# Kernel tuning notes

Measured on AMD Instinct MI355X. Metric: run time of the kernel, lower is better.

The kernel has to match this reference:

```python
import jax, jax.numpy as jnp
import numpy as np

HIDDEN = 1024
HEADS = 16
HEAD_DIM = HIDDEN // HEADS
B, T = 4, 2048


def setup_inputs() -> dict:
    key = jax.random.key(0)
    k_x, k_w1, k_b1, k_w2, k_b2 = jax.random.split(key, 5)
    lim1 = 1.0 / np.sqrt(HIDDEN)
    x = jax.random.normal(k_x, (B, T, HIDDEN), dtype=jnp.float32)
    # causal lower-triangular mask, broadcastable to [B, H, T, T]
    mask = jnp.tril(jnp.ones((T, T), dtype=jnp.int32))[None, None, :, :]
    # qkv_proj: Linear(HIDDEN, 3*HIDDEN); torch Linear: y = x @ W.T + b
    W_qkv = jax.random.uniform(k_w1, (3 * HIDDEN, HIDDEN), minval=-lim1, maxval=lim1, dtype=jnp.float32)
    b_qkv = jax.random.uniform(k_b1, (3 * HIDDEN,), minval=-lim1, maxval=lim1, dtype=jnp.float32)
    W_out = jax.random.uniform(k_w2, (HIDDEN, HIDDEN), minval=-lim1, maxval=lim1, dtype=jnp.float32)
    b_out = jax.random.uniform(k_b2, (HIDDEN,), minval=-lim1, maxval=lim1, dtype=jnp.float32)
    return {"x": x, "mask": mask, "W_qkv": W_qkv, "b_qkv": b_qkv, "W_out": W_out, "b_out": b_out}


def reference(x, mask, W_qkv, b_qkv, W_out, b_out):
    Bx, Tx, C = x.shape
    qkv = x @ W_qkv.T + b_qkv                      # [B, T, 3C]
    qkv = qkv.reshape(Bx, Tx, 3, HEADS, HEAD_DIM)
    qkv = jnp.transpose(qkv, (2, 0, 3, 1, 4))      # [3, B, H, T, Dh]
    Q, K, V = qkv[0], qkv[1], qkv[2]
    scale = 1.0 / np.sqrt(HEAD_DIM)
    scores = jnp.einsum('bhqd,bhkd->bhqk', Q, K) * scale  # [B, H, T, T]
    scores = jnp.where(mask == 0, -jnp.inf, scores)
    probs = jax.nn.softmax(scores, axis=-1)
    ctx = jnp.einsum('bhqk,bhkd->bhqd', probs, V)  # [B, H, T, Dh]
    ctx = jnp.transpose(ctx, (0, 2, 1, 3)).reshape(Bx, Tx, C)
    return ctx @ W_out.T + b_out
```

## Files before the change

### kernel.cpp

```cpp
#include <hip/hip_runtime.h>
#include <cstdint>
#include <cstddef>

#define B_ 4
#define T_ 2048
#define C_ 1024
#define H_ 16
#define D_ 64

typedef __attribute__((ext_vector_type(8))) __bf16 bf16x8;
typedef __attribute__((ext_vector_type(4))) float floatx4;

#define QSCL (0.125f * 1.44269504088896f)
#define FMAX 24.0f

__device__ __forceinline__ unsigned short f2bf(float f) {
  union { float f; unsigned int u; } v; v.f = f;
  unsigned int r = v.u + 0x7fffu + ((v.u >> 16) & 1u);
  return (unsigned short)(r >> 16);
}
__device__ __forceinline__ ushort4 pk4(float a, float b, float c, float d) {
  ushort4 u; u.x = f2bf(a); u.y = f2bf(b); u.z = f2bf(c); u.w = f2bf(d);
  return u;
}
__device__ __forceinline__ bf16x8 cvt8(float4 a, float4 b) {
  bf16x8 r;
  r[0] = a.x; r[1] = a.y; r[2] = a.z; r[3] = a.w;
  r[4] = b.x; r[5] = b.y; r[6] = b.z; r[7] = b.w;
  return r;
}
__device__ __forceinline__ unsigned pkbf2(float a, float b) {
  union { __bf16 h[2]; unsigned u; } w;
  w.h[0] = (__bf16)a; w.h[1] = (__bf16)b;
  return w.u;
}

__device__ __forceinline__ void gl_lds16(const void* g, void* l) {
  __builtin_amdgcn_global_load_lds(
      (const __attribute__((address_space(1))) unsigned int*)g,
      (__attribute__((address_space(3))) unsigned int*)l, 16, 0, 0);
}

__global__ __launch_bounds__(256)
void conv_bf16(const float* __restrict__ src, unsigned short* __restrict__ dst,
               int n8) {
  for (int i = blockIdx.x * 256 + threadIdx.x; i < n8; i += gridDim.x * 256) {
    const float4* s = (const float4*)src + 2 * (size_t)i;
    float4 a = s[0], b = s[1];
    ((bf16x8*)dst)[i] = cvt8(a, b);
  }
}

__global__ __launch_bounds__(256)
void conv_tri(const float* __restrict__ s1, unsigned short* __restrict__ d1, int n1,
              const float* __restrict__ s2, unsigned short* __restrict__ d2, int n2,
              const float* __restrict__ s3, unsigned short* __restrict__ d3, int n3) {
  for (int i = blockIdx.x * 256 + threadIdx.x; i < n1 + n2 + n3; i += gridDim.x * 256) {
    const float4* sp; bf16x8* dp;
    if (i < n1)           { sp = (const float4*)s1 + 2 * (size_t)i;       dp = (bf16x8*)d1 + i; }
    else if (i < n1 + n2) { int j = i - n1;      sp = (const float4*)s2 + 2 * (size_t)j; dp = (bf16x8*)d2 + j; }
    else                  { int j = i - n1 - n2; sp = (const float4*)s3 + 2 * (size_t)j; dp = (bf16x8*)d3 + j; }
    float4 a = sp[0], b = sp[1];
    *dp = cvt8(a, b);
  }
}

template<int EPI, int GATHER, int WBF>
__global__ __launch_bounds__(256, 2)
void gemm_bt(const unsigned short* __restrict__ Abf,
             const void* __restrict__ Wraw,
             const float* __restrict__ bias,
             float* __restrict__ out,
             unsigned short* __restrict__ qws,
             unsigned short* __restrict__ kws,
             unsigned short* __restrict__ vtws)
{
  alignas(16) __shared__ unsigned short As[2][128 * 64];
  alignas(16) __shared__ unsigned short Bs[2][WBF ? 128 * 64 : 128 * 72];
  const int tid  = threadIdx.x;
  const int lane = tid & 63;
  const int wid  = tid >> 6;
  const int col  = lane & 15;
  const int quad = lane >> 4;
  const int wm = (wid >> 1) << 6;
  const int wn = (wid & 1) << 6;
  const int bm = blockIdx.y << 7;
  const int bn = blockIdx.x << 7;

  const float* Wf          = (const float*)Wraw;
  const unsigned short* Wb = (const unsigned short*)Wraw;

  const int r0 = tid >> 3;
  const int c0 = tid & 7;

  floatx4 acc[4][4];
#pragma unroll
  for (int i = 0; i < 4; ++i)
#pragma unroll
    for (int j = 0; j < 4; ++j)
      acc[i][j] = (floatx4){0.f, 0.f, 0.f, 0.f};

#define GSTAGE(k0_, nb_)                                                      \
  do {                                                                        \
    _Pragma("unroll") for (int s = 0; s < 4; ++s) {                           \
      const int row  = (s << 5) + r0;                             \
      const int colE = ((c0 ^ (row & 7)) << 3);             \
      const unsigned short* gsrc;                                             \
      if (GATHER) {                                                           \
        const int m = bm + row;                                               \
        const int b = m >> 11, t = m & 2047;                                  \
        const int hh = (k0_) >> 6;                        \
        gsrc = Abf + ((((size_t)(b * 16 + hh) << 11) + t) << 6) + colE;       \
      } else {                                                                \
        gsrc = Abf + (size_t)(bm + row) * 1024 + (k0_) + colE;                \
      }                                                                       \
      gl_lds16(gsrc, (char*)&As[nb_][0] + (s << 12) + (wid << 10));           \
      if (WBF) {                                                              \
        const unsigned short* ws2 = Wb + (size_t)(bn + row) * 1024 + (k0_) + colE; \
        gl_lds16(ws2, (char*)&Bs[nb_][0] + (s << 12) + (wid << 10));          \
      } else {                                                                \
        const int kc = c0 << 3;                                               \
        const float* wsrc = &Wf[(size_t)(bn + row) * 1024 + (k0_) + kc];      \
        float4 w0 = *(const float4*)wsrc;                                     \
        float4 w1 = *(const float4*)(wsrc + 4);                               \
        *(bf16x8*)&Bs[nb_][row * 72 + kc] = cvt8(w0, w1);                     \
      }                                                                       \
    }                                                                         \
  } while (0)

  GSTAGE(0, 0);
  __syncthreads();

  for (int kt = 0; kt < 16; ++kt) {
    const int buf = kt & 1;
    if (kt + 1 < 16) GSTAGE((kt + 1) << 6, buf ^ 1);

#pragma unroll
    for (int kk = 0; kk < 64; kk += 32) {
      bf16x8 af[4], bfr[4];
#pragma unroll
      for (int i = 0; i < 4; ++i) {
        const int r = wm + i * 16 + col;
        af[i] = *(const bf16x8*)&As[buf][(r << 6) + ((kk + quad * 8) ^ ((r & 7) << 3))];
      }
#pragma unroll
      for (int j = 0; j < 4; ++j) {
        const int r = wn + j * 16 + col;
        if (WBF)
          bfr[j] = *(const bf16x8*)&Bs[buf][(r << 6) + ((kk + quad * 8) ^ ((r & 7) << 3))];
        else
          bfr[j] = *(const bf16x8*)&Bs[buf][r * 72 + kk + quad * 8];
      }
#pragma unroll
      for (int i = 0; i < 4; ++i)
#pragma unroll
        for (int j = 0; j < 4; ++j)
          acc[i][j] = __builtin_amdgcn_mfma_f32_16x16x32_bf16(af[i], bfr[j], acc[i][j], 0, 0, 0);
    }

    __syncthreads();
  }
#undef GSTAGE

#pragma unroll
  for (int i = 0; i < 4; ++i) {
    const int row = bm + wm + i * 16 + quad * 4;
#pragma unroll
    for (int j = 0; j < 4; ++j) {
      const int n  = bn + wn + j * 16 + col;
      const float bv = bias[n];
      float v[4];
#pragma unroll
      for (int r = 0; r < 4; ++r) v[r] = acc[i][j][r] + bv;

      if (EPI == 1) {
#pragma unroll
        for (int r = 0; r < 4; ++r)
          out[(size_t)(row + r) * 1024 + n] = v[r];
      } else {
        const int s   = n >> 10;
        const int rem = n & 1023;
        const int h   = rem >> 6;
        const int d   = rem & 63;
        const int b   = row >> 11;
        const int t   = row & 2047;
        const size_t bh = (size_t)(b * H_ + h);
        if (s == 0) {
#pragma unroll
          for (int r = 0; r < 4; ++r)
            qws[(bh * T_ + t + r) * D_ + d] = f2bf(v[r] * QSCL);
        } else if (s == 1) {
#pragma unroll
          for (int r = 0; r < 4; ++r)
            kws[(bh * T_ + t + r) * D_ + d] = f2bf(v[r]);
        } else {
          *(ushort4*)&vtws[(bh * D_ + d) * T_ + t] = pk4(v[0], v[1], v[2], v[3]);
        }
      }
    }
  }
}

__global__ __launch_bounds__(256, 2)
void attn_causal(unsigned short* __restrict__ qws,
                 const unsigned short* __restrict__ kws,
                 const unsigned short* __restrict__ vtws)
{
  alignas(16) __shared__ unsigned short Ks[2][64 * 64];
  alignas(16) __shared__ unsigned short Vs[2][64 * 64];
  const int tid  = threadIdx.x;
  const int lane = tid & 63;
  const int wid  = tid >> 6;
  const int col  = lane & 15;
  const int quad = lane >> 4;

  const int bh   = blockIdx.x & 63;
  const int band = 7 - (blockIdx.x >> 6);

  const unsigned short* Kp  = kws + (size_t)bh * T_ * D_;
  const unsigned short* Vtp = vtws + (size_t)bh * D_ * T_;

  bf16x8 vones;
#pragma unroll
  for (int i = 0; i < 8; ++i) vones[i] = (__bf16)1.0f;

  const int srow8 = lane >> 3;
  const int swz   = ((lane & 7) ^ srow8) << 3;

#define STAGE(kt_, b_)                                                        \
  do {                                                                        \
    _Pragma("unroll") for (int c2 = 0; c2 < 2; ++c2) {                        \
      const int cb = wid + (c2 << 2);                   \
      gl_lds16(Kp + ((size_t)(((kt_) << 6) + (cb << 3) + srow8) << 6) + swz,  \
               (char*)&Ks[b_][0] + (cb << 10));                               \
      gl_lds16(Vtp + ((size_t)((cb << 3) + srow8) << 11) + ((kt_) << 6) + swz,\
               (char*)&Vs[b_][0] + (cb << 10));                               \
    }                                                                         \
  } while (0)

  const int nk    = (band + 1) << 2;
  const int kdiag = (band << 2) + wid;
  const int q0    = (band << 8) + (wid << 6);
  unsigned short* Qp = qws + ((size_t)bh * T_ + q0) * D_;

  bf16x8 bq[4][2];
#pragma unroll
  for (int h = 0; h < 4; ++h) {
    bq[h][0] = *(const bf16x8*)&Qp[(h * 16 + col) * D_ + quad * 8];
    bq[h][1] = *(const bf16x8*)&Qp[(h * 16 + col) * D_ + 32 + quad * 8];
  }

  floatx4 o[4][4], ol[4];
#pragma unroll
  for (int h = 0; h < 4; ++h) {
    ol[h] = (floatx4){0.f, 0.f, 0.f, 0.f};
#pragma unroll
    for (int j = 0; j < 4; ++j) o[h][j] = (floatx4){0.f, 0.f, 0.f, 0.f};
  }

  STAGE(0, 0);
  __syncthreads();

  for (int kt = 0; kt < nk; ++kt) {
    const int buf = kt & 1;
    if (kt + 1 < nk) STAGE(kt + 1, buf ^ 1);

    if (kt <= kdiag) {
      const unsigned short* Kb = &Ks[buf][0];
      bf16x8 kA[4], kB[4];
#pragma unroll
      for (int g = 0; g < 4; ++g) {
        const int r = g * 16 + col;
        kA[g] = *(const bf16x8*)&Kb[(r << 6) + ((quad ^ (col & 7)) << 3)];
        kB[g] = *(const bf16x8*)&Kb[(r << 6) + (((quad | 4) ^ (col & 7)) << 3)];
      }
      const unsigned short* Vb = &Vs[buf][0];
      bf16x8 vA[4], vB[4];
#pragma unroll
      for (int j = 0; j < 4; ++j) {
        const int r = j * 16 + col;
        vA[j] = *(const bf16x8*)&Vb[(r << 6) + ((quad ^ (col & 7)) << 3)];
        vB[j] = *(const bf16x8*)&Vb[(r << 6) + (((quad | 4) ^ (col & 7)) << 3)];
      }

#pragma unroll
      for (int hp = 0; hp < 2; ++hp) {
        floatx4 s[2][4];
        __builtin_amdgcn_s_setprio(1);
#pragma unroll
        for (int hh = 0; hh < 2; ++hh) {
          const int h = hp * 2 + hh;
#pragma unroll
          for (int g = 0; g < 4; ++g) {
            s[hh][g] = (floatx4){-FMAX, -FMAX, -FMAX, -FMAX};
            s[hh][g] = __builtin_amdgcn_mfma_f32_16x16x32_bf16(kA[g], bq[h][0], s[hh][g], 0, 0, 0);
            s[hh][g] = __builtin_amdgcn_mfma_f32_16x16x32_bf16(kB[g], bq[h][1], s[hh][g], 0, 0, 0);
          }
        }
        __builtin_amdgcn_s_setprio(0);

        if (kt == kdiag) {
#pragma unroll
          for (int hh = 0; hh < 2; ++hh) {
            const int lim = ((hp * 2 + hh) << 4) + col;
#pragma unroll
            for (int g = 0; g < 4; ++g)
#pragma unroll
              for (int r = 0; r < 4; ++r)
                if (g * 16 + quad * 4 + r > lim) s[hh][g][r] = -1e30f;
          }
        }

#pragma unroll
        for (int hh = 0; hh < 2; ++hh)
#pragma unroll
          for (int g = 0; g < 4; ++g)
#pragma unroll
            for (int r = 0; r < 4; ++r)
              s[hh][g][r] = __builtin_amdgcn_exp2f(s[hh][g][r]);

        __builtin_amdgcn_s_setprio(1);
#pragma unroll
        for (int hh = 0; hh < 2; ++hh) {
          const int h = hp * 2 + hh;
          unsigned dw[4][2];
#pragma unroll
          for (int g = 0; g < 4; ++g) {
            dw[g][0] = pkbf2(s[hh][g][0], s[hh][g][1]);
            dw[g][1] = pkbf2(s[hh][g][2], s[hh][g][3]);
          }
          unsigned aw[4], bw[4];
          {
            auto t = __builtin_amdgcn_permlane32_swap(dw[0][0], dw[1][0], false, false);
            auto u = __builtin_amdgcn_permlane16_swap(t[0], t[1], false, false);
            aw[0] = u[0]; aw[2] = u[1];
          }
          {
            auto t = __builtin_amdgcn_permlane32_swap(dw[0][1], dw[1][1], false, false);
            auto u = __builtin_amdgcn_permlane16_swap(t[0], t[1], false, false);
            aw[1] = u[0]; aw[3] = u[1];
          }
          {
            auto t = __builtin_amdgcn_permlane32_swap(dw[2][0], dw[3][0], false, false);
            auto u = __builtin_amdgcn_permlane16_swap(t[0], t[1], false, false);
            bw[0] = u[0]; bw[2] = u[1];
          }
          {
            auto t = __builtin_amdgcn_permlane32_swap(dw[2][1], dw[3][1], false, false);
            auto u = __builtin_amdgcn_permlane16_swap(t[0], t[1], false, false);
            bw[1] = u[0]; bw[3] = u[1];
          }
          union { unsigned u[4]; bf16x8 v; } pa0, pa1;
#pragma unroll
          for (int w = 0; w < 4; ++w) { pa0.u[w] = aw[w]; pa1.u[w] = bw[w]; }

#pragma unroll
          for (int j = 0; j < 4; ++j) {
            o[h][j] = __builtin_amdgcn_mfma_f32_16x16x32_bf16(pa0.v, vA[j], o[h][j], 0, 0, 0);
            o[h][j] = __builtin_amdgcn_mfma_f32_16x16x32_bf16(pa1.v, vB[j], o[h][j], 0, 0, 0);
          }
          ol[h] = __builtin_amdgcn_mfma_f32_16x16x32_bf16(pa0.v, vones, ol[h], 0, 0, 0);
          ol[h] = __builtin_amdgcn_mfma_f32_16x16x32_bf16(pa1.v, vones, ol[h], 0, 0, 0);
        }
        __builtin_amdgcn_s_setprio(0);
      }
    }

    __syncthreads();
  }

#pragma unroll
  for (int h = 0; h < 4; ++h) {
    float lr[4];
#pragma unroll
    for (int r = 0; r < 4; ++r) lr[r] = 1.0f / ol[h][r];
#pragma unroll
    for (int j = 0; j < 4; ++j)
#pragma unroll
      for (int r = 0; r < 4; ++r)
        Qp[(size_t)(h * 16 + quad * 4 + r) * D_ + j * 16 + col] =
            f2bf(o[h][j][r] * lr[r]);
  }
#undef STAGE
}

extern "C" void kernel_launch(void* const* d_in, const int* in_sizes, int n_in,
                              void* d_out, int out_size, void* d_ws, size_t ws_size,
                              hipStream_t stream) {
  const float* x     = (const float*)d_in[0];
  const float* W_qkv = (const float*)d_in[2];
  const float* b_qkv = (const float*)d_in[3];
  const float* W_out = (const float*)d_in[4];
  const float* b_out = (const float*)d_in[5];
  float* out = (float*)d_out;

  const size_t per = (size_t)B_ * H_ * T_ * D_;
  unsigned short* qws  = (unsigned short*)d_ws;
  unsigned short* vtws = qws + per;
  unsigned short* kws  = (unsigned short*)d_out;
  unsigned short* xbf  = kws + per;

  const bool bigws  = ws_size >= (size_t)38 * 1024 * 1024;
  const bool hugews = ws_size >= (size_t)40 * 1024 * 1024;
  unsigned short* wqbf = vtws + per;
  unsigned short* wobf = wqbf + (size_t)3 * C_ * C_;

  if (hugews) {
    conv_tri<<<dim3(2048), 256, 0, stream>>>(
        x, xbf, (int)(per >> 3),
        W_qkv, wqbf, (3 * C_ * C_) >> 3,
        W_out, wobf, (C_ * C_) >> 3);
    gemm_bt<0, 0, 1><<<dim3(3072 / 128, 8192 / 128), 256, 0, stream>>>(
        xbf, (const void*)wqbf, b_qkv, nullptr, qws, kws, vtws);
  } else if (bigws) {
    conv_tri<<<dim3(2048), 256, 0, stream>>>(
        x, xbf, (int)(per >> 3),
        W_qkv, wqbf, (3 * C_ * C_) >> 3,
        nullptr, nullptr, 0);
    gemm_bt<0, 0, 1><<<dim3(3072 / 128, 8192 / 128), 256, 0, stream>>>(
        xbf, (const void*)wqbf, b_qkv, nullptr, qws, kws, vtws);
  } else {
    conv_bf16<<<dim3(2048), 256, 0, stream>>>(x, xbf, (int)(per >> 3));
    gemm_bt<0, 0, 0><<<dim3(3072 / 128, 8192 / 128), 256, 0, stream>>>(
        xbf, (const void*)W_qkv, b_qkv, nullptr, qws, kws, vtws);
  }

  attn_causal<<<dim3(8 * 64), 256, 0, stream>>>(qws, kws, vtws);

  if (hugews) {
    gemm_bt<1, 1, 1><<<dim3(1024 / 128, 8192 / 128), 256, 0, stream>>>(
        qws, (const void*)wobf, b_out, out, nullptr, nullptr, nullptr);
  } else {
    conv_bf16<<<dim3(512), 256, 0, stream>>>(W_out, vtws, (C_ * C_) >> 3);
    gemm_bt<1, 1, 1><<<dim3(1024 / 128, 8192 / 128), 256, 0, stream>>>(
        qws, (const void*)vtws, b_out, out, nullptr, nullptr, nullptr);
  }
}
```

Baseline: 261.9 us.

## Fuse conversion, QKV GEMM, attention and output GEMM into one cooperative kernel

Replaces the multi-launch pipeline with a single persistent cooperative kernel of 512 blocks that runs all stages in sequence, separated by grid-wide barriers, with shared memory unioned across phases. Attention is re-tiled into 128-row bands that are paired (band p with 15-p) to balance the causal workload per block. The aim is to remove kernel launch gaps and tail effects between stages. In exchange it adds grid.sync costs, fixes occupancy at two blocks per CU, and uses a smaller attention tile with less K/V reuse per block.

```diff
diff --git a/kernel.cpp b/kernel.cpp
--- a/kernel.cpp
+++ b/kernel.cpp
@@ -1,4 +1,5 @@
 #include <hip/hip_runtime.h>
+#include <hip/hip_cooperative_groups.h>
 #include <cstdint>
 #include <cstddef>
 
@@ -39,6 +40,350 @@
   __builtin_amdgcn_global_load_lds(
       (const __attribute__((address_space(1))) unsigned int*)g,
       (__attribute__((address_space(3))) unsigned int*)l, 16, 0, 0);
+}
+
+struct GemmSM { unsigned short As[2][8192]; unsigned short Bs[2][8192]; };
+struct AttnSM { unsigned short Ks[2][4096]; unsigned short Vs[2][4096]; };
+union FusedSM { GemmSM g; AttnSM a; };
+
+template<int EPI, int GATHER>
+__device__ __forceinline__ void gemm_body_w1(
+    const unsigned short* __restrict__ Abf,
+    const unsigned short* __restrict__ Wb,
+    const float* __restrict__ bias, float* __restrict__ out,
+    unsigned short* __restrict__ qws, unsigned short* __restrict__ kws,
+    unsigned short* __restrict__ vtws,
+    unsigned short* As, unsigned short* Bs, int bm, int bn)
+{
+  const int tid  = threadIdx.x;
+  const int lane = tid & 63;
+  const int wid  = tid >> 6;
+  const int col  = lane & 15;
+  const int quad = lane >> 4;
+  const int wm = (wid >> 1) << 6;
+  const int wn = (wid & 1) << 6;
+  const int r0 = tid >> 3;
+  const int c0 = tid & 7;
+
+  floatx4 acc[4][4];
+#pragma unroll
+  for (int i = 0; i < 4; ++i)
+#pragma unroll
+    for (int j = 0; j < 4; ++j)
+      acc[i][j] = (floatx4){0.f, 0.f, 0.f, 0.f};
+
+  auto stage = [&](int k0, int nb) {
+#pragma unroll
+    for (int s = 0; s < 4; ++s) {
+      const int row  = (s << 5) + r0;
+      const int colE = ((c0 ^ (row & 7)) << 3);
+      const unsigned short* gsrc;
+      if (GATHER) {
+        const int m = bm + row;
+        const int b = m >> 11, t = m & 2047;
+        const int hh = k0 >> 6;
+        gsrc = Abf + ((((size_t)(b * 16 + hh) << 11) + t) << 6) + colE;
+      } else {
+        gsrc = Abf + (size_t)(bm + row) * 1024 + k0 + colE;
+      }
+      gl_lds16(gsrc, (char*)As + nb * 16384 + (s << 12) + (wid << 10));
+      gl_lds16(Wb + (size_t)(bn + row) * 1024 + k0 + colE,
+               (char*)Bs + nb * 16384 + (s << 12) + (wid << 10));
+    }
+  };
+
+  stage(0, 0);
+  __syncthreads();
+
+  for (int kt = 0; kt < 16; ++kt) {
+    const int buf = kt & 1;
+    if (kt + 1 < 16) stage((kt + 1) << 6, buf ^ 1);
+#pragma unroll
+    for (int kk = 0; kk < 64; kk += 32) {
+      bf16x8 af[4], bfr[4];
+#pragma unroll
+      for (int i = 0; i < 4; ++i) {
+        const int r = wm + i * 16 + col;
+        af[i] = *(const bf16x8*)&As[buf * 8192 + (r << 6) + ((kk + quad * 8) ^ ((r & 7) << 3))];
+      }
+#pragma unroll
+      for (int j = 0; j < 4; ++j) {
+        const int r = wn + j * 16 + col;
+        bfr[j] = *(const bf16x8*)&Bs[buf * 8192 + (r << 6) + ((kk + quad * 8) ^ ((r & 7) << 3))];
+      }
+#pragma unroll
+      for (int i = 0; i < 4; ++i)
+#pragma unroll
+        for (int j = 0; j < 4; ++j)
+          acc[i][j] = __builtin_amdgcn_mfma_f32_16x16x32_bf16(af[i], bfr[j], acc[i][j], 0, 0, 0);
+    }
+    __syncthreads();
+  }
+
+#pragma unroll
+  for (int i = 0; i < 4; ++i) {
+    const int row = bm + wm + i * 16 + quad * 4;
+#pragma unroll
+    for (int j = 0; j < 4; ++j) {
+      const int n  = bn + wn + j * 16 + col;
+      const float bv = bias[n];
+      float v[4];
+#pragma unroll
+      for (int r = 0; r < 4; ++r) v[r] = acc[i][j][r] + bv;
+
+      if (EPI == 1) {
+#pragma unroll
+        for (int r = 0; r < 4; ++r)
+          out[(size_t)(row + r) * 1024 + n] = v[r];
+      } else {
+        const int s   = n >> 10;
+        const int rem = n & 1023;
+        const int h   = rem >> 6;
+        const int d   = rem & 63;
+        const int b   = row >> 11;
+        const int t   = row & 2047;
+        const size_t bh = (size_t)(b * H_ + h);
+        if (s == 0) {
+#pragma unroll
+          for (int r = 0; r < 4; ++r)
+            qws[(bh * T_ + t + r) * D_ + d] = f2bf(v[r] * QSCL);
+        } else if (s == 1) {
+#pragma unroll
+          for (int r = 0; r < 4; ++r)
+            kws[(bh * T_ + t + r) * D_ + d] = f2bf(v[r]);
+        } else {
+          *(ushort4*)&vtws[(bh * D_ + d) * T_ + t] = pk4(v[0], v[1], v[2], v[3]);
+        }
+      }
+    }
+  }
+}
+
+__global__ __launch_bounds__(256, 2)
+void fused_all(const float* __restrict__ x,
+               const float* __restrict__ Wq,
+               const float* __restrict__ bqv,
+               const float* __restrict__ Wo,
+               const float* __restrict__ bov,
+               float* __restrict__ out,
+               unsigned short* __restrict__ qws,
+               unsigned short* __restrict__ vtws,
+               unsigned short* __restrict__ kws,
+               unsigned short* __restrict__ xbf,
+               unsigned short* __restrict__ wqbf)
+{
+  __shared__ FusedSM sm;
+  cooperative_groups::grid_group grid = cooperative_groups::this_grid();
+  const int tid  = threadIdx.x;
+  const int lane = tid & 63;
+  const int wid  = tid >> 6;
+  const int col  = lane & 15;
+  const int quad = lane >> 4;
+
+  {
+    const int n1 = 1048576;
+    const int n2 = 393216;
+    for (int i = (int)blockIdx.x * 256 + tid; i < n1 + n2; i += 512 * 256) {
+      if (i < n1) {
+        const float4* s = (const float4*)x + 2 * (size_t)i;
+        ((bf16x8*)xbf)[i] = cvt8(s[0], s[1]);
+      } else {
+        const int j = i - n1;
+        const float4* s = (const float4*)Wq + 2 * (size_t)j;
+        ((bf16x8*)wqbf)[j] = cvt8(s[0], s[1]);
+      }
+    }
+  }
+  grid.sync();
+
+  for (int t5 = 0; t5 < 3; ++t5) {
+    const int tile = (int)blockIdx.x + (t5 << 9);
+    const int by = tile / 24, bx = tile - by * 24;
+    gemm_body_w1<0, 0>(xbf, wqbf, bqv, nullptr, qws, kws, vtws,
+                       &sm.g.As[0][0], &sm.g.Bs[0][0], by << 7, bx << 7);
+  }
+  grid.sync();
+
+  {
+    unsigned short* Kls = &sm.a.Ks[0][0];
+    unsigned short* Vls = &sm.a.Vs[0][0];
+    const int bh = (int)blockIdx.x & 63;
+    const int p  = (int)blockIdx.x >> 6;
+    const unsigned short* Kp  = kws + (size_t)bh * T_ * D_;
+    const unsigned short* Vtp = vtws + (size_t)bh * D_ * T_;
+
+    bf16x8 vones;
+#pragma unroll
+    for (int i = 0; i < 8; ++i) vones[i] = (__bf16)1.0f;
+
+    const int srow8 = lane >> 3;
+    const int aswz  = ((lane & 7) ^ srow8) << 3;
+    auto astage = [&](int kt_, int b_) {
+#pragma unroll
+      for (int c2 = 0; c2 < 2; ++c2) {
+        const int cb = wid + (c2 << 2);
+        gl_lds16(Kp + ((size_t)((kt_ << 6) + (cb << 3) + srow8) << 6) + aswz,
+                 (char*)Kls + b_ * 8192 + (cb << 10));
+        gl_lds16(Vtp + ((size_t)((cb << 3) + srow8) << 11) + (kt_ << 6) + aswz,
+                 (char*)Vls + b_ * 8192 + (cb << 10));
+      }
+    };
+
+    for (int half = 0; half < 2; ++half) {
+      const int band = half ? (15 - p) : p;
+      const int nk   = (band << 1) + 2;
+      const int q0   = (band << 7) + (wid << 5);
+      unsigned short* Qp = qws + ((size_t)bh * T_ + q0) * D_;
+
+      bf16x8 bq[2][2];
+#pragma unroll
+      for (int h = 0; h < 2; ++h) {
+        bq[h][0] = *(const bf16x8*)&Qp[(h * 16 + col) * D_ + quad * 8];
+        bq[h][1] = *(const bf16x8*)&Qp[(h * 16 + col) * D_ + 32 + quad * 8];
+      }
+
+      floatx4 o[2][4], ol[2];
+#pragma unroll
+      for (int h = 0; h < 2; ++h) {
+        ol[h] = (floatx4){0.f, 0.f, 0.f, 0.f};
+#pragma unroll
+        for (int j = 0; j < 4; ++j) o[h][j] = (floatx4){0.f, 0.f, 0.f, 0.f};
+      }
+
+      astage(0, 0);
+      __syncthreads();
+
+      for (int kt = 0; kt < nk; ++kt) {
+        const int buf = kt & 1;
+        if (kt + 1 < nk) astage(kt + 1, buf ^ 1);
+
+        const unsigned short* Kb = Kls + buf * 4096;
+        bf16x8 kA[4], kB[4];
+#pragma unroll
+        for (int g = 0; g < 4; ++g) {
+          const int r = g * 16 + col;
+          kA[g] = *(const bf16x8*)&Kb[(r << 6) + ((quad ^ (col & 7)) << 3)];
+          kB[g] = *(const bf16x8*)&Kb[(r << 6) + (((quad | 4) ^ (col & 7)) << 3)];
+        }
+
+        floatx4 s[2][4];
+        __builtin_amdgcn_s_setprio(1);
+#pragma unroll
+        for (int h = 0; h < 2; ++h)
+#pragma unroll
+          for (int g = 0; g < 4; ++g) {
+            s[h][g] = (floatx4){-FMAX, -FMAX, -FMAX, -FMAX};
+            s[h][g] = __builtin_amdgcn_mfma_f32_16x16x32_bf16(kA[g], bq[h][0], s[h][g], 0, 0, 0);
+            s[h][g] = __builtin_amdgcn_mfma_f32_16x16x32_bf16(kB[g], bq[h][1], s[h][g], 0, 0, 0);
+          }
+        __builtin_amdgcn_s_setprio(0);
+
+        const unsigned short* Vb = Vls + buf * 4096;
+        bf16x8 vA[4], vB[4];
+#pragma unroll
+        for (int j = 0; j < 4; ++j) {
+          const int r = j * 16 + col;
+          vA[j] = *(const bf16x8*)&Vb[(r << 6) + ((quad ^ (col & 7)) << 3)];
+          vB[j] = *(const bf16x8*)&Vb[(r << 6) + (((quad | 4) ^ (col & 7)) << 3)];
+        }
+
+        if (kt >= nk - 2) {
+#pragma unroll
+          for (int h = 0; h < 2; ++h) {
+            const int lim = q0 - (kt << 6) + (h << 4) + col;
+#pragma unroll
+            for (int g = 0; g < 4; ++g)
+#pragma unroll
+              for (int r = 0; r < 4; ++r)
+                if (g * 16 + quad * 4 + r > lim) s[h][g][r] = -1e30f;
+          }
+        }
+
+#pragma unroll
+        for (int h = 0; h < 2; ++h)
+#pragma unroll
+          for (int g = 0; g < 4; ++g)
+#pragma unroll
+            for (int r = 0; r < 4; ++r)
+              s[h][g][r] = __builtin_amdgcn_exp2f(s[h][g][r]);
+
+        __builtin_amdgcn_s_setprio(1);
+#pragma unroll
+        for (int h = 0; h < 2; ++h) {
+          unsigned dw[4][2];
+#pragma unroll
+          for (int g = 0; g < 4; ++g) {
+            dw[g][0] = pkbf2(s[h][g][0], s[h][g][1]);
+            dw[g][1] = pkbf2(s[h][g][2], s[h][g][3]);
+          }
+          unsigned aw[4], bw[4];
+          {
+            auto t = __builtin_amdgcn_permlane32_swap(dw[0][0], dw[1][0], false, false);
+            auto u = __builtin_amdgcn_permlane16_swap(t[0], t[1], false, false);
+            aw[0] = u[0]; aw[2] = u[1];
+          }
+          {
+            auto t = __builtin_amdgcn_permlane32_swap(dw[0][1], dw[1][1], false, false);
+            auto u = __builtin_amdgcn_permlane16_swap(t[0], t[1], false, false);
+            aw[1] = u[0]; aw[3] = u[1];
+          }
+          {
+            auto t = __builtin_amdgcn_permlane32_swap(dw[2][0], dw[3][0], false, false);
+            auto u = __builtin_amdgcn_permlane16_swap(t[0], t[1], false, false);
+            bw[0] = u[0]; bw[2] = u[1];
+          }
+          {
+            auto t = __builtin_amdgcn_permlane32_swap(dw[2][1], dw[3][1], false, false);
+            auto u = __builtin_amdgcn_permlane16_swap(t[0], t[1], false, false);
+            bw[1] = u[0]; bw[3] = u[1];
+          }
+          union { unsigned u[4]; bf16x8 v; } pa0, pa1;
+#pragma unroll
+          for (int w = 0; w < 4; ++w) { pa0.u[w] = aw[w]; pa1.u[w] = bw[w]; }
+
+#pragma unroll
+          for (int j = 0; j < 4; ++j) {
+            o[h][j] = __builtin_amdgcn_mfma_f32_16x16x32_bf16(pa0.v, vA[j], o[h][j], 0, 0, 0);
+            o[h][j] = __builtin_amdgcn_mfma_f32_16x16x32_bf16(pa1.v, vB[j], o[h][j], 0, 0, 0);
+          }
+          ol[h] = __builtin_amdgcn_mfma_f32_16x16x32_bf16(pa0.v, vones, ol[h], 0, 0, 0);
+          ol[h] = __builtin_amdgcn_mfma_f32_16x16x32_bf16(pa1.v, vones, ol[h], 0, 0, 0);
+        }
+        __builtin_amdgcn_s_setprio(0);
+
+        __syncthreads();
+      }
+
+#pragma unroll
+      for (int h = 0; h < 2; ++h) {
+        float lr[4];
+#pragma unroll
+        for (int r = 0; r < 4; ++r) lr[r] = 1.0f / ol[h][r];
+#pragma unroll
+        for (int j = 0; j < 4; ++j)
+#pragma unroll
+          for (int r = 0; r < 4; ++r)
+            Qp[(size_t)(h * 16 + quad * 4 + r) * D_ + j * 16 + col] =
+                f2bf(o[h][j][r] * lr[r]);
+      }
+    }
+  }
+  grid.sync();
+
+  {
+    for (int i = (int)blockIdx.x * 256 + tid; i < 131072; i += 512 * 256) {
+      const float4* s = (const float4*)Wo + 2 * (size_t)i;
+      ((bf16x8*)vtws)[i] = cvt8(s[0], s[1]);
+    }
+  }
+  grid.sync();
+
+  {
+    const int tile = (int)blockIdx.x;
+    const int by = tile >> 3, bx = tile & 7;
+    gemm_body_w1<1, 1>(qws, vtws, bov, out, nullptr, nullptr, nullptr,
+                       &sm.g.As[0][0], &sm.g.Bs[0][0], by << 7, bx << 7);
+  }
 }
 
 __global__ __launch_bounds__(256)
@@ -103,13 +448,13 @@
 #define GSTAGE(k0_, nb_)                                                      \
   do {                                                                        \
     _Pragma("unroll") for (int s = 0; s < 4; ++s) {                           \
-      const int row  = (s << 5) + r0;                             \
-      const int colE = ((c0 ^ (row & 7)) << 3);             \
+      const int row  = (s << 5) + r0;                                         \
+      const int colE = ((c0 ^ (row & 7)) << 3);                               \
       const unsigned short* gsrc;                                             \
       if (GATHER) {                                                           \
         const int m = bm + row;                                               \
         const int b = m >> 11, t = m & 2047;                                  \
-        const int hh = (k0_) >> 6;                        \
+        const int hh = (k0_) >> 6;                                            \
         gsrc = Abf + ((((size_t)(b * 16 + hh) << 11) + t) << 6) + colE;       \
       } else {                                                                \
         gsrc = Abf + (size_t)(bm + row) * 1024 + (k0_) + colE;                \
@@ -157,7 +502,6 @@
         for (int j = 0; j < 4; ++j)
           acc[i][j] = __builtin_amdgcn_mfma_f32_16x16x32_bf16(af[i], bfr[j], acc[i][j], 0, 0, 0);
     }
-
     __syncthreads();
   }
 #undef GSTAGE
@@ -230,7 +574,7 @@
 #define STAGE(kt_, b_)                                                        \
   do {                                                                        \
     _Pragma("unroll") for (int c2 = 0; c2 < 2; ++c2) {                        \
-      const int cb = wid + (c2 << 2);                   \
+      const int cb = wid + (c2 << 2);                                         \
       gl_lds16(Kp + ((size_t)(((kt_) << 6) + (cb << 3) + srow8) << 6) + swz,  \
                (char*)&Ks[b_][0] + (cb << 10));                               \
       gl_lds16(Vtp + ((size_t)((cb << 3) + srow8) << 11) + ((kt_) << 6) + swz,\
@@ -365,7 +709,6 @@
         __builtin_amdgcn_s_setprio(0);
       }
     }
-
     __syncthreads();
   }
 
@@ -404,6 +747,20 @@
   const bool hugews = ws_size >= (size_t)40 * 1024 * 1024;
   unsigned short* wqbf = vtws + per;
   unsigned short* wobf = wqbf + (size_t)3 * C_ * C_;
+
+  if (bigws) {
+    int dev = 0, coop = 0;
+    hipGetDevice(&dev);
+    hipDeviceGetAttribute(&coop, hipDeviceAttributeCooperativeLaunch, dev);
+    if (coop) {
+      void* args[] = {(void*)&x, (void*)&W_qkv, (void*)&b_qkv, (void*)&W_out,
+                      (void*)&b_out, (void*)&out, (void*)&qws, (void*)&vtws,
+                      (void*)&kws, (void*)&xbf, (void*)&wqbf};
+      if (hipLaunchCooperativeKernel((void*)fused_all, dim3(512), dim3(256),
+                                     args, 0, stream) == hipSuccess)
+        return;
+    }
+  }
 
   if (hugews) {
     conv_tri<<<dim3(2048), 256, 0, stream>>>(
```

Result: slower. 504.3 us (+92.6%).

## Add 4-stage BK=32 pipelined GEMM with fine-grained vmcnt waits for projections

Applied to the files above, without the earlier changes.

Adds a new bf16 GEMM kernel that uses a K tile of 32 and a four-buffer LDS ring. Loads are issued three stages ahead, and each iteration waits only on the oldest batch with explicit vmcnt waits and a raw s_barrier, instead of a full __syncthreads per 64-wide K step. MFMA issue runs at raised priority. The QKV and output projections use this kernel when the workspace is large enough. The goal is to hide global-to-LDS latency better; in exchange it runs more barriers and smaller MFMA batches per iteration.

```diff
diff --git a/kernel.cpp b/kernel.cpp
--- a/kernel.cpp
+++ b/kernel.cpp
@@ -62,6 +62,133 @@
     else                  { int j = i - n1 - n2; sp = (const float4*)s3 + 2 * (size_t)j; dp = (bf16x8*)d3 + j; }
     float4 a = sp[0], b = sp[1];
     *dp = cvt8(a, b);
+  }
+}
+
+template<int EPI, int GATHER>
+__global__ __launch_bounds__(256, 2)
+void gemm32(const unsigned short* __restrict__ Abf,
+            const unsigned short* __restrict__ Wb,
+            const float* __restrict__ bias,
+            float* __restrict__ out,
+            unsigned short* __restrict__ qws,
+            unsigned short* __restrict__ kws,
+            unsigned short* __restrict__ vtws)
+{
+  alignas(16) __shared__ unsigned short As[4][128 * 32];
+  alignas(16) __shared__ unsigned short Bs[4][128 * 32];
+  const int tid  = threadIdx.x;
+  const int lane = tid & 63;
+  const int wid  = tid >> 6;
+  const int col  = lane & 15;
+  const int quad = lane >> 4;
+  const int wm = (wid >> 1) << 6;
+  const int wn = (wid & 1) << 6;
+  const int bm = blockIdx.y << 7;
+  const int bn = blockIdx.x << 7;
+
+  floatx4 acc[4][4];
+#pragma unroll
+  for (int i = 0; i < 4; ++i)
+#pragma unroll
+    for (int j = 0; j < 4; ++j)
+      acc[i][j] = (floatx4){0.f, 0.f, 0.f, 0.f};
+
+  auto stage = [&](int k0, int nb) {
+#pragma unroll
+    for (int q2 = 0; q2 < 2; ++q2) {
+      const int rloc = (((wid << 1) | q2) << 4) + (lane >> 2);
+      const int swc  = (lane & 3) ^ ((rloc >> 1) & 3);
+      const char* dstA = (char*)&As[nb][0] + (((wid << 1) | q2) << 10);
+      const char* dstB = (char*)&Bs[nb][0] + (((wid << 1) | q2) << 10);
+      const unsigned short* ga;
+      if (GATHER) {
+        const int m = bm + rloc;
+        const int b = m >> 11, t = m & 2047;
+        const int hh = k0 >> 6;
+        const int d  = (k0 & 63) + (swc << 3);
+        ga = Abf + ((((size_t)(b * 16 + hh) << 11) + t) << 6) + d;
+      } else {
+        ga = Abf + (size_t)(bm + rloc) * 1024 + k0 + (swc << 3);
+      }
+      gl_lds16(ga, (void*)dstA);
+      gl_lds16(Wb + (size_t)(bn + rloc) * 1024 + k0 + (swc << 3), (void*)dstB);
+    }
+  };
+
+  stage(0, 0);
+  stage(32, 1);
+  stage(64, 2);
+  asm volatile("s_waitcnt vmcnt(8)" ::: "memory");
+  __builtin_amdgcn_s_barrier();
+  __builtin_amdgcn_sched_barrier(0);
+
+  for (int kt = 0; kt < 32; ++kt) {
+    const int buf = kt & 3;
+    if (kt + 3 < 32) stage((kt + 3) << 5, (kt + 3) & 3);
+
+    bf16x8 af[4], bfr[4];
+#pragma unroll
+    for (int i = 0; i < 4; ++i) {
+      const int r = wm + i * 16 + col;
+      af[i] = *(const bf16x8*)&As[buf][(r << 5) + ((quad ^ ((r >> 1) & 3)) << 3)];
+    }
+#pragma unroll
+    for (int j = 0; j < 4; ++j) {
+      const int r = wn + j * 16 + col;
+      bfr[j] = *(const bf16x8*)&Bs[buf][(r << 5) + ((quad ^ ((r >> 1) & 3)) << 3)];
+    }
+    __builtin_amdgcn_s_setprio(1);
+#pragma unroll
+    for (int i = 0; i < 4; ++i)
+#pragma unroll
+      for (int j = 0; j < 4; ++j)
+        acc[i][j] = __builtin_amdgcn_mfma_f32_16x16x32_bf16(af[i], bfr[j], acc[i][j], 0, 0, 0);
+    __builtin_amdgcn_s_setprio(0);
+
+    if (kt < 29)       { asm volatile("s_waitcnt vmcnt(8)" ::: "memory"); }
+    else if (kt == 29) { asm volatile("s_waitcnt vmcnt(4)" ::: "memory"); }
+    else if (kt == 30) { asm volatile("s_waitcnt vmcnt(0)" ::: "memory"); }
+    __builtin_amdgcn_s_barrier();
+    __builtin_amdgcn_sched_barrier(0);
+  }
+
+#pragma unroll
+  for (int i = 0; i < 4; ++i) {
+    const int row = bm + wm + i * 16 + quad * 4;
+#pragma unroll
+    for (int j = 0; j < 4; ++j) {
+      const int n  = bn + wn + j * 16 + col;
+      const float bv = bias[n];
+      float v[4];
+#pragma unroll
+      for (int r = 0; r < 4; ++r) v[r] = acc[i][j][r] + bv;
+
+      if (EPI == 1) {
+#pragma unroll
+        for (int r = 0; r < 4; ++r)
+          out[(size_t)(row + r) * 1024 + n] = v[r];
+      } else {
+        const int s   = n >> 10;
+        const int rem = n & 1023;
+        const int h   = rem >> 6;
+        const int d   = rem & 63;
+        const int b   = row >> 11;
+        const int t   = row & 2047;
+        const size_t bh = (size_t)(b * H_ + h);
+        if (s == 0) {
+#pragma unroll
+          for (int r = 0; r < 4; ++r)
+            qws[(bh * T_ + t + r) * D_ + d] = f2bf(v[r] * QSCL);
+        } else if (s == 1) {
+#pragma unroll
+          for (int r = 0; r < 4; ++r)
+            kws[(bh * T_ + t + r) * D_ + d] = f2bf(v[r]);
+        } else {
+          *(ushort4*)&vtws[(bh * D_ + d) * T_ + t] = pk4(v[0], v[1], v[2], v[3]);
+        }
+      }
+    }
   }
 }
 
@@ -103,13 +230,13 @@
 #define GSTAGE(k0_, nb_)                                                      \
   do {                                                                        \
     _Pragma("unroll") for (int s = 0; s < 4; ++s) {                           \
-      const int row  = (s << 5) + r0;                             \
-      const int colE = ((c0 ^ (row & 7)) << 3);             \
+      const int row  = (s << 5) + r0;                                         \
+      const int colE = ((c0 ^ (row & 7)) << 3);                               \
       const unsigned short* gsrc;                                             \
       if (GATHER) {                                                           \
         const int m = bm + row;                                               \
         const int b = m >> 11, t = m & 2047;                                  \
-        const int hh = (k0_) >> 6;                        \
+        const int hh = (k0_) >> 6;                                            \
         gsrc = Abf + ((((size_t)(b * 16 + hh) << 11) + t) << 6) + colE;       \
       } else {                                                                \
         gsrc = Abf + (size_t)(bm + row) * 1024 + (k0_) + colE;                \
@@ -157,7 +284,6 @@
         for (int j = 0; j < 4; ++j)
           acc[i][j] = __builtin_amdgcn_mfma_f32_16x16x32_bf16(af[i], bfr[j], acc[i][j], 0, 0, 0);
     }
-
     __syncthreads();
   }
 #undef GSTAGE
@@ -230,7 +356,7 @@
 #define STAGE(kt_, b_)                                                        \
   do {                                                                        \
     _Pragma("unroll") for (int c2 = 0; c2 < 2; ++c2) {                        \
-      const int cb = wid + (c2 << 2);                   \
+      const int cb = wid + (c2 << 2);                                         \
       gl_lds16(Kp + ((size_t)(((kt_) << 6) + (cb << 3) + srow8) << 6) + swz,  \
                (char*)&Ks[b_][0] + (cb << 10));                               \
       gl_lds16(Vtp + ((size_t)((cb << 3) + srow8) << 11) + ((kt_) << 6) + swz,\
@@ -365,7 +491,6 @@
         __builtin_amdgcn_s_setprio(0);
       }
     }
-
     __syncthreads();
   }
 
@@ -410,15 +535,15 @@
         x, xbf, (int)(per >> 3),
         W_qkv, wqbf, (3 * C_ * C_) >> 3,
         W_out, wobf, (C_ * C_) >> 3);
-    gemm_bt<0, 0, 1><<<dim3(3072 / 128, 8192 / 128), 256, 0, stream>>>(
-        xbf, (const void*)wqbf, b_qkv, nullptr, qws, kws, vtws);
+    gemm32<0, 0><<<dim3(3072 / 128, 8192 / 128), 256, 0, stream>>>(
+        xbf, wqbf, b_qkv, nullptr, qws, kws, vtws);
   } else if (bigws) {
     conv_tri<<<dim3(2048), 256, 0, stream>>>(
         x, xbf, (int)(per >> 3),
         W_qkv, wqbf, (3 * C_ * C_) >> 3,
         nullptr, nullptr, 0);
-    gemm_bt<0, 0, 1><<<dim3(3072 / 128, 8192 / 128), 256, 0, stream>>>(
-        xbf, (const void*)wqbf, b_qkv, nullptr, qws, kws, vtws);
+    gemm32<0, 0><<<dim3(3072 / 128, 8192 / 128), 256, 0, stream>>>(
+        xbf, wqbf, b_qkv, nullptr, qws, kws, vtws);
   } else {
     conv_bf16<<<dim3(2048), 256, 0, stream>>>(x, xbf, (int)(per >> 3));
     gemm_bt<0, 0, 0><<<dim3(3072 / 128, 8192 / 128), 256, 0, stream>>>(
@@ -428,8 +553,12 @@
   attn_causal<<<dim3(8 * 64), 256, 0, stream>>>(qws, kws, vtws);
 
   if (hugews) {
-    gemm_bt<1, 1, 1><<<dim3(1024 / 128, 8192 / 128), 256, 0, stream>>>(
-        qws, (const void*)wobf, b_out, out, nullptr, nullptr, nullptr);
+    gemm32<1, 1><<<dim3(1024 / 128, 8192 / 128), 256, 0, stream>>>(
+        qws, wobf, b_out, out, nullptr, nullptr, nullptr);
+  } else if (bigws) {
+    conv_bf16<<<dim3(512), 256, 0, stream>>>(W_out, vtws, (C_ * C_) >> 3);
+    gemm32<1, 1><<<dim3(1024 / 128, 8192 / 128), 256, 0, stream>>>(
+        qws, vtws, b_out, out, nullptr, nullptr, nullptr);
   } else {
     conv_bf16<<<dim3(512), 256, 0, stream>>>(W_out, vtws, (C_ * C_) >> 3);
     gemm_bt<1, 1, 1><<<dim3(1024 / 128, 8192 / 128), 256, 0, stream>>>(
```

Measured after the change: 281.2 us. 1.07x slower.
